# Optimization experiments

Measured on AMD Instinct MI355X. Metric: run time of the kernel, lower is better.

## Reference

```python
import jax, jax.numpy as jnp
import numpy as np
from jax import lax

B, C, L = 32, 8, 4096
K, S = 128, 64  # num_shapelets, shapelets_size


def setup_inputs() -> dict:
    key = jax.random.key(0)
    kx, ks = jax.random.split(key)
    x = jax.random.normal(kx, (B, C, L), dtype=jnp.float32)
    shapelets = jax.random.normal(ks, (C, K, S), dtype=jnp.float32)
    return {"x": x, "shapelets": shapelets}


def reference(x, shapelets):
    # x: (B, C, L); shapelets: (C, K, S)
    # Equivalent to: unfold -> cdist(p=2) -> sum over channels -> min over windows.
    # Use the ||a-b||^2 = ||a||^2 + ||b||^2 - 2 a.b expansion so the unfolded
    # (B, C, W, S) tensor is never materialized; cross-terms via grouped conv.
    Bc, Cc, Lc = x.shape
    _, Kc, Sc = shapelets.shape
    dn = ("NCH", "OIH", "NCH")
    # cross[b, c*K+k, w] = sum_s x[b,c,w+s] * shapelets[c,k,s]
    rhs = shapelets.reshape(Cc * Kc, 1, Sc)
    cross = lax.conv_general_dilated(x, rhs, (1,), "VALID",
                                     feature_group_count=Cc,
                                     dimension_numbers=dn)  # (B, C*K, W)
    W = cross.shape[-1]
    cross = cross.reshape(Bc, Cc, Kc, W)
    # sliding window squared norms of x: conv of x^2 with ones kernel per channel
    ones = jnp.ones((Cc, 1, Sc), x.dtype)
    xnorm = lax.conv_general_dilated(x * x, ones, (1,), "VALID",
                                     feature_group_count=Cc,
                                     dimension_numbers=dn)  # (B, C, W)
    snorm = jnp.sum(shapelets * shapelets, axis=-1)  # (C, K)
    d2 = xnorm[:, :, None, :] + snorm[None, :, :, None] - 2.0 * cross  # (B,C,K,W)
    d = jnp.sqrt(jnp.maximum(d2, 1e-12))
    summed = jnp.sum(d, axis=1, keepdims=True)  # (B, 1, K, W)
    return jnp.min(summed, axis=3)  # (B, 1, K)
```

## Files before the change

### kernel.cpp

```cpp
#include <hip/hip_runtime.h>


typedef short short8 __attribute__((ext_vector_type(8)));
typedef float f32x4 __attribute__((ext_vector_type(4)));

constexpr int Bn = 32, Cn = 8, Ln = 4096, Kn = 128, Sn = 64;
constexpr int Wn = Ln - Sn + 1;
constexpr int WT = 128;
constexpr int NWT = (Wn + WT - 1) / WT;
constexpr int BDIM = 256;

__device__ __forceinline__ unsigned int f2bf(float f) {
  unsigned int u = __float_as_uint(f);
  u += 0x7FFFu + ((u >> 16) & 1u);
  return u >> 16;
}

__global__ void prep_kernel(const float* __restrict__ sh,
                            unsigned int* __restrict__ out,
                            unsigned short* __restrict__ hbf,
                            float* __restrict__ snorm) {
  int gid = blockIdx.x * blockDim.x + threadIdx.x;
  out[gid] = 0x7F7FFFFFu;
  if (gid < Cn * Kn) {
    const float4* row = (const float4*)(sh + (size_t)gid * Sn);
    uint2* orow = (uint2*)(hbf + (size_t)gid * Sn);
    float a = 0.f;
    #pragma unroll
    for (int i = 0; i < 16; ++i) {
      float4 v = row[i];
      a += v.x * v.x + v.y * v.y + v.z * v.z + v.w * v.w;
      unsigned int p0 = f2bf(-2.f * v.x) | (f2bf(-2.f * v.y) << 16);
      unsigned int p1 = f2bf(-2.f * v.z) | (f2bf(-2.f * v.w) << 16);
      orow[i] = make_uint2(p0, p1);
    }
    snorm[gid] = a;
  }
}

__launch_bounds__(BDIM, 2)
__global__ void med_kernel(const float* __restrict__ x,
                           const unsigned short* __restrict__ hbf,
                           const float* __restrict__ snorm,
                           unsigned int* __restrict__ out) {
  constexpr int XRS = 200;
  constexpr int BSS = 80;
  __shared__ __align__(16) unsigned short Xr[8 * XRS];
  __shared__ __align__(16) unsigned short Bs[Kn * BSS];
  __shared__ __align__(16) float xnormC[Cn * WT];
  __shared__ __align__(16) float snormC[Cn * Kn];

  const int tid  = threadIdx.x;
  const int b    = blockIdx.y;
  const int w0   = blockIdx.x * WT;
  const int lane = tid & 63;
  const int wv   = tid >> 6;
  const int quad = lane >> 4;
  const int n16  = lane & 15;
  const int wbase = wv * 32;

  const float* xb = x + (size_t)b * Cn * Ln;

  ((float4*)snormC)[tid] = ((const float4*)snorm)[tid];

  {
    int c  = tid >> 5;
    int m0 = (tid & 31) * 4;
    const float* xc = xb + c * Ln;
    auto xq = [&](int i) -> float {
      float v = (i < Ln) ? xc[i] : 0.f;
      return v * v;
    };
    float s0 = 0.f;
    for (int s = 0; s < Sn; ++s) s0 += xq(w0 + m0 + s);
    float s1 = s0 - xq(w0 + m0 + 0) + xq(w0 + m0 + 64);
    float s2 = s1 - xq(w0 + m0 + 1) + xq(w0 + m0 + 65);
    float s3 = s2 - xq(w0 + m0 + 2) + xq(w0 + m0 + 66);
    xnormC[c * WT + m0 + 0] = s0;
    xnormC[c * WT + m0 + 1] = s1;
    xnormC[c * WT + m0 + 2] = s2;
    xnormC[c * WT + m0 + 3] = s3;
  }

  float dist[2][8][4] = {};

  for (int c = 0; c < Cn; ++c) {
    __syncthreads();

    {
      const float* xc = xb + c * Ln;
      #pragma unroll
      for (int rep = 0; rep < 3; ++rep) {
        int pid = tid + rep * BDIM;
        int r = pid / 96;
        int p = pid - r * 96;
        int i0 = w0 + r + 2 * p;
        float f0 = (i0 < Ln) ? xc[i0] : 0.f;
        float f1 = (i0 + 1 < Ln) ? xc[i0 + 1] : 0.f;
        *(unsigned int*)(&Xr[r * XRS + 2 * p]) = f2bf(f0) | (f2bf(f1) << 16);
      }
    }
    {
      const uint4* hb = (const uint4*)(hbf + (size_t)c * Kn * Sn);
      #pragma unroll
      for (int rep = 0; rep < 4; ++rep) {
        int qid = tid + rep * BDIM;
        int k = qid >> 3, ch = qid & 7;
        *(uint4*)(&Bs[k * BSS + ch * 8]) = hb[qid];
      }
    }
    __syncthreads();

    float4 xn[2];
    #pragma unroll
    for (int mt = 0; mt < 2; ++mt)
      xn[mt] = *(const float4*)(&xnormC[c * WT + wbase + mt * 16 + quad * 4]);

    short8 af[2][2];
    #pragma unroll
    for (int mt = 0; mt < 2; ++mt)
      #pragma unroll
      for (int ks = 0; ks < 2; ++ks) {
        int i = wbase + mt * 16 + n16 + ks * 32 + quad * 8;
        af[mt][ks] = *(const short8*)(&Xr[(i & 7) * XRS + (i >> 3) * 8]);
      }

    #pragma unroll
    for (int pass = 0; pass < 2; ++pass) {
      short8 bfr[4][2];
      float sn[4];
      #pragma unroll
      for (int nt = 0; nt < 4; ++nt) {
        int ksh = pass * 64 + nt * 16 + n16;
        sn[nt] = snormC[c * Kn + ksh];
        #pragma unroll
        for (int ks = 0; ks < 2; ++ks)
          bfr[nt][ks] = *(const short8*)(&Bs[ksh * BSS + ks * 32 + quad * 8]);
      }
      #pragma unroll
      for (int mt = 0; mt < 2; ++mt)
        #pragma unroll
        for (int nt = 0; nt < 4; ++nt) {
          f32x4 acc;
          #pragma unroll
          for (int rg = 0; rg < 4; ++rg) acc[rg] = xn[mt][rg] + sn[nt];
          acc = __builtin_amdgcn_mfma_f32_16x16x32_bf16(af[mt][0], bfr[nt][0], acc, 0, 0, 0);
          acc = __builtin_amdgcn_mfma_f32_16x16x32_bf16(af[mt][1], bfr[nt][1], acc, 0, 0, 0);
          #pragma unroll
          for (int rg = 0; rg < 4; ++rg)
            dist[mt][pass * 4 + nt][rg] += __builtin_amdgcn_sqrtf(acc[rg]);
        }
    }
  }

  const int wql = w0 + wbase + quad * 4;
  #pragma unroll
  for (int nt2 = 0; nt2 < 8; ++nt2) {
    float v = 3.4e38f;
    #pragma unroll
    for (int mt = 0; mt < 2; ++mt)
      #pragma unroll
      for (int rg = 0; rg < 4; ++rg) {
        int wg = wql + mt * 16 + rg;
        float d = (wg < Wn) ? dist[mt][nt2][rg] : 3.4e38f;
        v = fminf(v, d);
      }
    v = fminf(v, __shfl_xor(v, 16, 64));
    v = fminf(v, __shfl_xor(v, 32, 64));
    if (lane < 16)
      atomicMin(&out[b * Kn + nt2 * 16 + n16], __float_as_uint(v));
  }
}

extern "C" void kernel_launch(void* const* d_in, const int* in_sizes, int n_in,
                              void* d_out, int out_size, void* d_ws, size_t ws_size,
                              hipStream_t stream) {
  const float* x  = (const float*)d_in[0];
  const float* sh = (const float*)d_in[1];
  unsigned int* out = (unsigned int*)d_out;
  unsigned short* hbf = (unsigned short*)d_ws;
  float* snorm = (float*)((char*)d_ws + (size_t)Cn * Kn * Sn * 2);
  hipLaunchKernelGGL(prep_kernel, dim3(16), dim3(256), 0, stream, sh, out, hbf, snorm);
  hipLaunchKernelGGL(med_kernel, dim3(NWT, Bn), dim3(BDIM), 0, stream, x, hbf, snorm, out);
}
```

Measured before the change: 113.0 us.

## Prefetch next-channel shapelets into registers, raise occupancy, reduce mins in LDS

Shapelet bf16 tiles for the next channel are loaded into registers during the current channel's MFMA work and written to LDS at the start of the next iteration, overlapping global latency with compute. The launch bound is raised to 4 blocks per SM and per-block minima are first combined in shared memory, so only one global atomic per k per block is issued. In exchange, register pressure rises (Breg plus the higher occupancy target), which risks spills.

```diff
diff --git a/kernel.cpp b/kernel.cpp
--- a/kernel.cpp
+++ b/kernel.cpp
@@ -38,7 +38,7 @@
   }
 }
 
-__launch_bounds__(BDIM, 2)
+__launch_bounds__(BDIM, 4)
 __global__ void med_kernel(const float* __restrict__ x,
                            const unsigned short* __restrict__ hbf,
                            const float* __restrict__ snorm,
@@ -49,6 +49,7 @@
   __shared__ __align__(16) unsigned short Bs[Kn * BSS];
   __shared__ __align__(16) float xnormC[Cn * WT];
   __shared__ __align__(16) float snormC[Cn * Kn];
+  __shared__ unsigned int smin[Kn];
 
   const int tid  = threadIdx.x;
   const int b    = blockIdx.y;
@@ -62,6 +63,7 @@
   const float* xb = x + (size_t)b * Cn * Ln;
 
   ((float4*)snormC)[tid] = ((const float4*)snorm)[tid];
+  if (tid < Kn) smin[tid] = 0x7F7FFFFFu;
 
   {
     int c  = tid >> 5;
@@ -82,34 +84,47 @@
     xnormC[c * WT + m0 + 3] = s3;
   }
 
+  const uint4* hb4 = (const uint4*)hbf;
+  const int bk = tid >> 3, bch = tid & 7;
+  uint4 Breg[4];
+  #pragma unroll
+  for (int rep = 0; rep < 4; ++rep) Breg[rep] = hb4[tid + rep * BDIM];
+
   float dist[2][8][4] = {};
 
   for (int c = 0; c < Cn; ++c) {
     __syncthreads();
 
-    {
-      const float* xc = xb + c * Ln;
-      #pragma unroll
-      for (int rep = 0; rep < 3; ++rep) {
-        int pid = tid + rep * BDIM;
-        int r = pid / 96;
-        int p = pid - r * 96;
-        int i0 = w0 + r + 2 * p;
-        float f0 = (i0 < Ln) ? xc[i0] : 0.f;
-        float f1 = (i0 + 1 < Ln) ? xc[i0 + 1] : 0.f;
-        *(unsigned int*)(&Xr[r * XRS + 2 * p]) = f2bf(f0) | (f2bf(f1) << 16);
-      }
-    }
-    {
-      const uint4* hb = (const uint4*)(hbf + (size_t)c * Kn * Sn);
-      #pragma unroll
-      for (int rep = 0; rep < 4; ++rep) {
-        int qid = tid + rep * BDIM;
-        int k = qid >> 3, ch = qid & 7;
-        *(uint4*)(&Bs[k * BSS + ch * 8]) = hb[qid];
-      }
-    }
+    const float* xc = xb + c * Ln;
+    float xf[3][2];
+    int pid0 = tid;
+    #pragma unroll
+    for (int rep = 0; rep < 3; ++rep) {
+      int pid = tid + rep * BDIM;
+      int r = pid / 96;
+      int p = pid - r * 96;
+      int i0 = w0 + r + 2 * p;
+      xf[rep][0] = (i0 < Ln) ? xc[i0] : 0.f;
+      xf[rep][1] = (i0 + 1 < Ln) ? xc[i0 + 1] : 0.f;
+    }
+    #pragma unroll
+    for (int rep = 0; rep < 4; ++rep)
+      *(uint4*)(&Bs[(bk + rep * 32) * BSS + bch * 8]) = Breg[rep];
+    #pragma unroll
+    for (int rep = 0; rep < 3; ++rep) {
+      int pid = tid + rep * BDIM;
+      int r = pid / 96;
+      int p = pid - r * 96;
+      *(unsigned int*)(&Xr[r * XRS + 2 * p]) = f2bf(xf[rep][0]) | (f2bf(xf[rep][1]) << 16);
+    }
+    (void)pid0;
     __syncthreads();
+
+    if (c < Cn - 1) {
+      #pragma unroll
+      for (int rep = 0; rep < 4; ++rep)
+        Breg[rep] = hb4[(c + 1) * 1024 + tid + rep * BDIM];
+    }
 
     float4 xn[2];
     #pragma unroll
@@ -168,8 +183,11 @@
     v = fminf(v, __shfl_xor(v, 16, 64));
     v = fminf(v, __shfl_xor(v, 32, 64));
     if (lane < 16)
-      atomicMin(&out[b * Kn + nt2 * 16 + n16], __float_as_uint(v));
-  }
+      atomicMin(&smin[nt2 * 16 + n16], __float_as_uint(v));
+  }
+  __syncthreads();
+  if (tid < Kn)
+    atomicMin(&out[b * Kn + tid], smin[tid]);
 }
 
 extern "C" void kernel_launch(void* const* d_in, const int* in_sizes, int n_in,
```

Measured after the change: 264.1 us. 134% more time.
